# Kernel tuning notes

Hardware: AMD Instinct MI355X
Metric: run time of the kernel (lower is better)

Reference implementation:

```python
import jax, jax.numpy as jnp
import numpy as np

TEMP = 0.5  # temperature from init_kwargs
EPS = 1e-8  # torch.nn.CosineSimilarity eps


def setup_inputs() -> dict:
    key = jax.random.key(0)
    k1, k2 = jax.random.split(key)
    B, D = 4096, 128
    return {
        "z_i": jax.random.normal(k1, (B, D), dtype=jnp.float32),
        "z_j": jax.random.normal(k2, (B, D), dtype=jnp.float32),
    }


def reference(z_i, z_j):
    B = z_i.shape[0]          # batch_size * world_size
    N = 2 * B
    z = jnp.concatenate([z_i, z_j], axis=0)              # [N, D]
    zn = z / jnp.maximum(jnp.linalg.norm(z, axis=1, keepdims=True), EPS)
    sim = (zn @ zn.T) / TEMP                             # [N, N] cosine sim / temp
    # positives: sim[i, i+B] and sim[i+B, i]
    pos = jnp.concatenate([jnp.diagonal(sim, offset=B), jnp.diagonal(sim, offset=-B)])  # [N]
    # CE with label 0 over [pos, negatives]; since the positive-pair entry equals pos,
    # denominator = sum_{j != i} exp(sim[i, j])  (only the diagonal is excluded)
    eye = jnp.eye(N, dtype=bool)
    sim_masked = jnp.where(eye, -jnp.inf, sim)
    lse = jax.nn.logsumexp(sim_masked, axis=1)           # [N]
    loss = jnp.sum(lse - pos) / N                        # reduction='sum' then /= N
    return loss
```

## Files before the change

kernel.cpp:

```cpp
#include <hip/hip_runtime.h>
#include <hip/hip_bf16.h>


typedef short bfrag __attribute__((ext_vector_type(8)));
typedef float f32x4 __attribute__((ext_vector_type(4)));

static __device__ __forceinline__ unsigned short f2bf_rne(float x) {
    unsigned u = __float_as_uint(x);
    return (unsigned short)((u + 0x7fffu + ((u >> 16) & 1u)) >> 16);
}
static __device__ __forceinline__ float bf2f(unsigned short b) {
    return __uint_as_float(((unsigned)b) << 16);
}

__global__ __launch_bounds__(256) void nt_norm_pair(
        const float* __restrict__ zi, const float* __restrict__ zj,
        unsigned short* __restrict__ zn, float* __restrict__ diag,
        float* __restrict__ pos, float* __restrict__ sumexp) {
    constexpr int B = 4096, D = 128;
    const int wave = threadIdx.x >> 6, lane = threadIdx.x & 63;
    const int p = blockIdx.x * 4 + wave;
    float2 a = reinterpret_cast<const float2*>(zi + (size_t)p * D)[lane];
    float2 b = reinterpret_cast<const float2*>(zj + (size_t)p * D)[lane];
    float sa = a.x * a.x + a.y * a.y;
    float sb = b.x * b.x + b.y * b.y;
    #pragma unroll
    for (int m = 32; m; m >>= 1) { sa += __shfl_xor(sa, m); sb += __shfl_xor(sb, m); }
    float ia = 1.f / fmaxf(sqrtf(sa), 1e-8f);
    float ib = 1.f / fmaxf(sqrtf(sb), 1e-8f);
    unsigned short a0 = f2bf_rne(a.x * ia), a1 = f2bf_rne(a.y * ia);
    unsigned short b0 = f2bf_rne(b.x * ib), b1 = f2bf_rne(b.y * ib);
    float fa0 = bf2f(a0), fa1 = bf2f(a1), fb0 = bf2f(b0), fb1 = bf2f(b1);
    float da = fa0 * fa0 + fa1 * fa1;
    float db = fb0 * fb0 + fb1 * fb1;
    float cr = fa0 * fb0 + fa1 * fb1;
    #pragma unroll
    for (int m = 32; m; m >>= 1) {
        da += __shfl_xor(da, m); db += __shfl_xor(db, m); cr += __shfl_xor(cr, m);
    }
    reinterpret_cast<unsigned*>(zn + (size_t)p * D)[lane] =
        (unsigned)a0 | ((unsigned)a1 << 16);
    reinterpret_cast<unsigned*>(zn + (size_t)(p + B) * D)[lane] =
        (unsigned)b0 | ((unsigned)b1 << 16);
    if (lane == 0) {
        diag[p] = da; diag[p + B] = db;
        pos[p] = 2.f * cr; pos[p + B] = 2.f * cr;
        sumexp[p] = 0.f; sumexp[p + B] = 0.f;
    }
}

__global__ __launch_bounds__(256, 4) void nt_gram_sym(
        const unsigned short* __restrict__ zn, float* __restrict__ sumexp) {
    const int c = blockIdx.x;
    const int y = blockIdx.y;
    if (y == 16 && c >= 64) return;
    const int T  = (y == 16) ? 1 : 4;
    const int d0 = (y == 16) ? 64 : 4 * y;

    __shared__ short buf[2][64][128];

    const short* zs = (const short*)zn;
    const int tid = threadIdx.x, wid = tid >> 6, lane = tid & 63;
    const int wj = wid >> 1, wi = wid & 1;
    const int lr = lane & 15, lk = lane >> 4;

    bfrag ca[4][2];
    {
        const int rbase = c * 64 + wj * 32;
        #pragma unroll
        for (int ks = 0; ks < 4; ++ks)
            #pragma unroll
            for (int f = 0; f < 2; ++f)
                ca[ks][f] = *reinterpret_cast<const bfrag*>(
                    zs + (size_t)(rbase + f * 16 + lr) * 128 + ks * 32 + lk * 8);
    }

    auto STAGE = [&](int t, int slot) {
        const int srow = ((c + d0 + t) & 127) * 64;
        #pragma unroll
        for (int q = 0; q < 4; ++q) {
            const int cbase = q * 256 + wid * 64;
            const int chunk = cbase + lane;
            const int r = chunk >> 4;
            const int cpos = chunk & 15;
            const int csrc = cpos ^ (r & 7);
            const short* g = zs + (size_t)(srow + r) * 128 + csrc * 8;
            __builtin_amdgcn_global_load_lds(
                (const __attribute__((address_space(1))) void*)g,
                (__attribute__((address_space(3))) void*)(
                    &buf[slot][0][0] + (size_t)cbase * 8),
                16, 0, 0);
        }
    };

    STAGE(0, 0);

    constexpr float K_E = 2.8853900817779268f;
    float jp[8] = {0.f, 0.f, 0.f, 0.f, 0.f, 0.f, 0.f, 0.f};

    for (int t = 0; t < T; ++t) {
        if (t + 1 < T) {
            STAGE(t + 1, (t + 1) & 1);
            asm volatile("s_waitcnt vmcnt(4)" ::: "memory");
        } else {
            asm volatile("s_waitcnt vmcnt(0)" ::: "memory");
        }
        __builtin_amdgcn_s_barrier();

        const int sb = ((c + d0 + t) & 127) * 64;
        f32x4 acc[2][2] = {};
        #pragma unroll
        for (int ks = 0; ks < 4; ++ks) {
            bfrag cb[2];
            #pragma unroll
            for (int f = 0; f < 2; ++f) {
                const int r = wi * 32 + f * 16 + lr;
                const int cc = (ks * 4 + lk) ^ (lr & 7);
                cb[f] = *reinterpret_cast<const bfrag*>(&buf[t & 1][r][cc * 8]);
            }
            #pragma unroll
            for (int fj = 0; fj < 2; ++fj)
                #pragma unroll
                for (int fi = 0; fi < 2; ++fi)
                    acc[fj][fi] = __builtin_amdgcn_mfma_f32_16x16x32_bf16(
                        ca[ks][fj], cb[fi], acc[fj][fi], 0, 0, 0);
        }

        const float cw = (d0 + t) ? 1.f : 0.f;
        #pragma unroll
        for (int fi = 0; fi < 2; ++fi) {
            float s = 0.f;
            #pragma unroll
            for (int fj = 0; fj < 2; ++fj)
                #pragma unroll
                for (int r = 0; r < 4; ++r) {
                    const float e = exp2f(acc[fj][fi][r] * K_E);
                    s += e;
                    jp[fj * 4 + r] += e * cw;
                }
            s += __shfl_xor(s, 16);
            s += __shfl_xor(s, 32);
            if (lk == 0) atomicAdd(&sumexp[sb + wi * 32 + fi * 16 + lr], s);
        }
        __builtin_amdgcn_s_barrier();
    }

    float myv = 0.f;
    #pragma unroll
    for (int tt = 0; tt < 8; ++tt) {
        float v = jp[tt];
        v += __shfl_xor(v, 1);
        v += __shfl_xor(v, 2);
        v += __shfl_xor(v, 4);
        v += __shfl_xor(v, 8);
        if (lr == tt) myv = v;
    }
    if (lr < 8)
        atomicAdd(&sumexp[c * 64 + wj * 32 + (lr >> 2) * 16 + lk * 4 + (lr & 3)], myv);
}

__global__ __launch_bounds__(1024) void nt_finalize(
        const float* __restrict__ sumexp, const float* __restrict__ diag,
        const float* __restrict__ pos, float* __restrict__ out) {
    constexpr int N = 8192;
    constexpr float K_E = 2.8853900817779268f;
    float s = 0.f;
    for (int i = threadIdx.x; i < N; i += 1024)
        s += __logf(sumexp[i] - exp2f(diag[i] * K_E)) - pos[i];
    #pragma unroll
    for (int m = 32; m; m >>= 1) s += __shfl_xor(s, m);
    __shared__ float red[16];
    if ((threadIdx.x & 63) == 0) red[threadIdx.x >> 6] = s;
    __syncthreads();
    if (threadIdx.x == 0) {
        float t = 0.f;
        #pragma unroll
        for (int w = 0; w < 16; ++w) t += red[w];
        out[0] = t * (1.0f / (float)N);
    }
}

extern "C" void kernel_launch(void* const* d_in, const int* in_sizes, int n_in,
                              void* d_out, int out_size, void* d_ws, size_t ws_size,
                              hipStream_t stream) {
    const float* zi = (const float*)d_in[0];
    const float* zj = (const float*)d_in[1];
    float* out = (float*)d_out;

    char* ws = (char*)d_ws;
    unsigned short* zn = (unsigned short*)ws;
    float* sumexp = (float*)(ws + 2 * 1024 * 1024);
    float* diag   = (float*)(ws + 2 * 1024 * 1024 + 1 * 32768);
    float* pos    = (float*)(ws + 2 * 1024 * 1024 + 2 * 32768);

    nt_norm_pair<<<1024, 256, 0, stream>>>(zi, zj, zn, diag, pos, sumexp);
    nt_gram_sym<<<dim3(128, 17), 256, 0, stream>>>(zn, sumexp);
    nt_finalize<<<1, 1024, 0, stream>>>(sumexp, diag, pos, out);
}
```

Before: 36.42 us.

## Fuse finalize into gram kernel via last-block counter and double tiles per block

Removes the separate finalize launch. An atomic completion counter now lets the last gram block compute the loss reduction, and the counter is reset by the norm kernel. Each block now processes 8 column tiles instead of 4, which halves the grid and amortises the A-fragment loads, and the waitcnt logic is adjusted for the extra outstanding atomics. The risks are a serial tail in the last block, fewer blocks for load balance, and reliance on the exact active-block count.

```diff
diff --git a/kernel.cpp b/kernel.cpp
--- a/kernel.cpp
+++ b/kernel.cpp
@@ -16,7 +16,8 @@
 __global__ __launch_bounds__(256) void nt_norm_pair(
         const float* __restrict__ zi, const float* __restrict__ zj,
         unsigned short* __restrict__ zn, float* __restrict__ diag,
-        float* __restrict__ pos, float* __restrict__ sumexp) {
+        float* __restrict__ pos, float* __restrict__ sumexp,
+        int* __restrict__ done) {
     constexpr int B = 4096, D = 128;
     const int wave = threadIdx.x >> 6, lane = threadIdx.x & 63;
     const int p = blockIdx.x * 4 + wave;
@@ -47,17 +48,23 @@
         pos[p] = 2.f * cr; pos[p + B] = 2.f * cr;
         sumexp[p] = 0.f; sumexp[p + B] = 0.f;
     }
-}
-
+    if (blockIdx.x == 0 && threadIdx.x == 0) *done = 0;
+}
+
+#define NACTIVE 1088
 __global__ __launch_bounds__(256, 4) void nt_gram_sym(
-        const unsigned short* __restrict__ zn, float* __restrict__ sumexp) {
+        const unsigned short* __restrict__ zn, float* __restrict__ sumexp,
+        const float* __restrict__ diag, const float* __restrict__ pos,
+        int* __restrict__ done, float* __restrict__ out) {
     const int c = blockIdx.x;
     const int y = blockIdx.y;
-    if (y == 16 && c >= 64) return;
-    const int T  = (y == 16) ? 1 : 4;
-    const int d0 = (y == 16) ? 64 : 4 * y;
+    if (y == 8 && c >= 64) return;
+    const int T  = (y == 8) ? 1 : 8;
+    const int d0 = (y == 8) ? 64 : 8 * y;
 
     __shared__ short buf[2][64][128];
+    __shared__ float red[4];
+    __shared__ int lastFlag;
 
     const short* zs = (const short*)zn;
     const int tid = threadIdx.x, wid = tid >> 6, lane = tid & 63;
@@ -74,6 +81,7 @@
                 ca[ks][f] = *reinterpret_cast<const bfrag*>(
                     zs + (size_t)(rbase + f * 16 + lr) * 128 + ks * 32 + lk * 8);
     }
+    asm volatile("s_waitcnt vmcnt(0)" ::: "memory");
 
     auto STAGE = [&](int t, int slot) {
         const int srow = ((c + d0 + t) & 127) * 64;
@@ -99,11 +107,14 @@
     float jp[8] = {0.f, 0.f, 0.f, 0.f, 0.f, 0.f, 0.f, 0.f};
 
     for (int t = 0; t < T; ++t) {
-        if (t + 1 < T) {
-            STAGE(t + 1, (t + 1) & 1);
-            asm volatile("s_waitcnt vmcnt(4)" ::: "memory");
+        const bool more = (t + 1 < T);
+        if (more) STAGE(t + 1, (t + 1) & 1);
+        if (t == 0) {
+            if (more) asm volatile("s_waitcnt vmcnt(4)" ::: "memory");
+            else      asm volatile("s_waitcnt vmcnt(0)" ::: "memory");
         } else {
-            asm volatile("s_waitcnt vmcnt(0)" ::: "memory");
+            if (more) asm volatile("s_waitcnt vmcnt(6)" ::: "memory");
+            else      asm volatile("s_waitcnt vmcnt(2)" ::: "memory");
         }
         __builtin_amdgcn_s_barrier();
 
@@ -157,27 +168,31 @@
     }
     if (lr < 8)
         atomicAdd(&sumexp[c * 64 + wj * 32 + (lr >> 2) * 16 + lk * 4 + (lr & 3)], myv);
-}
-
-__global__ __launch_bounds__(1024) void nt_finalize(
-        const float* __restrict__ sumexp, const float* __restrict__ diag,
-        const float* __restrict__ pos, float* __restrict__ out) {
+
+    __threadfence();
+    __syncthreads();
+    if (tid == 0) {
+        int v = __hip_atomic_fetch_add(done, 1, __ATOMIC_ACQ_REL,
+                                       __HIP_MEMORY_SCOPE_AGENT);
+        lastFlag = (v == NACTIVE - 1);
+    }
+    __syncthreads();
+    if (!lastFlag) return;
+
+    __threadfence();
     constexpr int N = 8192;
-    constexpr float K_E = 2.8853900817779268f;
     float s = 0.f;
-    for (int i = threadIdx.x; i < N; i += 1024)
-        s += __logf(sumexp[i] - exp2f(diag[i] * K_E)) - pos[i];
+    for (int i = tid; i < N; i += 256) {
+        float se = __hip_atomic_load(&sumexp[i], __ATOMIC_RELAXED,
+                                     __HIP_MEMORY_SCOPE_AGENT);
+        s += __logf(se - exp2f(diag[i] * K_E)) - pos[i];
+    }
     #pragma unroll
     for (int m = 32; m; m >>= 1) s += __shfl_xor(s, m);
-    __shared__ float red[16];
-    if ((threadIdx.x & 63) == 0) red[threadIdx.x >> 6] = s;
+    if (lane == 0) red[wid] = s;
     __syncthreads();
-    if (threadIdx.x == 0) {
-        float t = 0.f;
-        #pragma unroll
-        for (int w = 0; w < 16; ++w) t += red[w];
-        out[0] = t * (1.0f / (float)N);
-    }
+    if (tid == 0)
+        out[0] = (red[0] + red[1] + red[2] + red[3]) * (1.0f / (float)N);
 }
 
 extern "C" void kernel_launch(void* const* d_in, const int* in_sizes, int n_in,
@@ -192,8 +207,8 @@
     float* sumexp = (float*)(ws + 2 * 1024 * 1024);
     float* diag   = (float*)(ws + 2 * 1024 * 1024 + 1 * 32768);
     float* pos    = (float*)(ws + 2 * 1024 * 1024 + 2 * 32768);
-
-    nt_norm_pair<<<1024, 256, 0, stream>>>(zi, zj, zn, diag, pos, sumexp);
-    nt_gram_sym<<<dim3(128, 17), 256, 0, stream>>>(zn, sumexp);
-    nt_finalize<<<1, 1024, 0, stream>>>(sumexp, diag, pos, out);
-}
+    int*   done   = (int*)  (ws + 2 * 1024 * 1024 + 3 * 32768);
+
+    nt_norm_pair<<<1024, 256, 0, stream>>>(zi, zj, zn, diag, pos, sumexp, done);
+    nt_gram_sym<<<dim3(128, 9), 256, 0, stream>>>(zn, sumexp, diag, pos, done, out);
+}
```

Measured after the change: 116.8 us. 221% more time.
